# Performance work log

Measured on AMD Instinct MI355X. Metric: run time of the kernel, lower is better.

Reference implementation:

```python
import jax, jax.numpy as jnp
import numpy as np

N_NODES = 50000
N_EDGES = 800000
IN_FEAT = 128
OUT_FEAT = 128


def _glorot(key, shape):
    fan_in, fan_out = shape[1], shape[0]
    lim = jnp.sqrt(6.0 / (fan_in + fan_out))
    return jax.random.uniform(key, shape, jnp.float32, -lim, lim)


def setup_inputs() -> dict:
    key = jax.random.key(0)
    ks = jax.random.split(key, 9)
    x = jax.random.normal(ks[0], (N_NODES, IN_FEAT), jnp.float32)
    edge_index = jax.random.randint(ks[1], (2, N_EDGES), 0, N_NODES, jnp.int64)
    # SAGEConv params: lin_l applied to aggregated neighbors (with bias),
    # lin_r applied to root features (no bias) -- PyG default mean aggregation.
    W1l = _glorot(ks[2], (OUT_FEAT, IN_FEAT)); b1l = jnp.zeros((OUT_FEAT,), jnp.float32)
    W1r = _glorot(ks[3], (OUT_FEAT, IN_FEAT))
    W2l = _glorot(ks[4], (OUT_FEAT, OUT_FEAT)); b2l = jnp.zeros((OUT_FEAT,), jnp.float32)
    W2r = _glorot(ks[5], (OUT_FEAT, OUT_FEAT))
    Wlin = _glorot(ks[6], (2, OUT_FEAT)); blin = jnp.zeros((2,), jnp.float32)
    return {"x": x, "edge_index": edge_index,
            "W1l": W1l, "b1l": b1l, "W1r": W1r,
            "W2l": W2l, "b2l": b2l, "W2r": W2r,
            "Wlin": Wlin, "blin": blin}


def _sage_conv(x, src, dst, Wl, bl, Wr, n_nodes):
    # mean-aggregate neighbor features at destination nodes
    agg_sum = jax.ops.segment_sum(x[src], dst, num_segments=n_nodes)  # [N, F]
    deg = jax.ops.segment_sum(jnp.ones((src.shape[0],), x.dtype), dst, num_segments=n_nodes)
    agg = agg_sum / jnp.maximum(deg, 1.0)[:, None]
    return agg @ Wl.T + bl + x @ Wr.T


def reference(x, edge_index, W1l, b1l, W1r, W2l, b2l, W2r, Wlin, blin):
    src, dst = edge_index[0], edge_index[1]
    n = x.shape[0]
    h = _sage_conv(x, src, dst, W1l, b1l, W1r, n)
    h = jax.nn.relu(h)  # dropout is identity in eval mode
    h = _sage_conv(h, src, dst, W2l, b2l, W2r, n)
    h = jax.nn.relu(h)
    logits = h @ Wlin.T + blin  # [N, 2]
    return jax.nn.log_softmax(logits, axis=1)
```

## Files before the change

### kernel.cpp

```cpp
#include <hip/hip_runtime.h>
#include <math.h>

#define N_NODES 50000
#define N_EDGES 800000
#define F 128
#define ELL_CAP 64
#define NSHARD 8
#define RANKS 128
#define EPR (N_EDGES / RANKS)
#define NPS (N_NODES / NSHARD)
#define NBPS 25
#define NBUCK (NSHARD * NBPS)
#define BIN_CAP 80
#define BUCK_CAP 4608
#define EDGE_BLKS (NSHARD * RANKS)
#define CVT_BLKS 6250

typedef __attribute__((ext_vector_type(8))) short short8;
typedef __attribute__((ext_vector_type(4))) float float4v;

__device__ inline unsigned short f2bf(float f) {
    unsigned int u = __builtin_bit_cast(unsigned int, f);
    u += 0x7FFF + ((u >> 16) & 1);
    return (unsigned short)(u >> 16);
}
__device__ inline float bf2f_lo(unsigned int u) {
    return __builtin_bit_cast(float, u << 16);
}
__device__ inline float bf2f_hi(unsigned int u) {
    return __builtin_bit_cast(float, u & 0xFFFF0000u);
}
__device__ inline float i8f(unsigned int u, int k) {
    return (float)((signed char)(u >> (k * 8)));
}

__global__ __launch_bounds__(256) void prep1(const float* __restrict__ x,
                                             const int* __restrict__ src,
                                             const int* __restrict__ dst,
                                             const float* __restrict__ W1l,
                                             const float* __restrict__ W1r,
                                             const float* __restrict__ W2l,
                                             const float* __restrict__ W2r,
                                             unsigned short* __restrict__ xb,
                                             unsigned char* __restrict__ xq,
                                             float* __restrict__ xscale,
                                             int* __restrict__ tails,
                                             unsigned int* __restrict__ bucketEdges,
                                             unsigned short* __restrict__ P1,
                                             unsigned short* __restrict__ P2) {
    int blk = blockIdx.x;
    int tid = threadIdx.x;
    if (blk < EDGE_BLKS) {
        __shared__ int bin_cnt[NBPS];
        __shared__ int bin_base[NBPS];
        __shared__ unsigned int bins[NBPS * BIN_CAP];
        int shard = blk & 7;
        int rank = blk >> 3;
        int lo = shard * NPS;
        if (tid < NBPS) bin_cnt[tid] = 0;
        __syncthreads();
        int base = rank * EPR;
        for (int i = tid; i < EPR; i += 256) {
            int d = dst[base + i];
            unsigned int du = (unsigned int)(d - lo);
            if (du < (unsigned int)NPS) {
                int s = src[base + i];
                int lb = du >> 8;
                int pos = atomicAdd(&bin_cnt[lb], 1);
                if (pos < BIN_CAP)
                    bins[lb * BIN_CAP + pos] = ((du & 255u) << 16) | (unsigned int)s;
            }
        }
        __syncthreads();
        if (tid < NBPS) {
            int c = bin_cnt[tid]; if (c > BIN_CAP) c = BIN_CAP;
            bin_cnt[tid] = c;
            bin_base[tid] = atomicAdd(&tails[shard * NBPS + tid], c);
        }
        __syncthreads();
        for (int b2 = 0; b2 < NBPS; ++b2) {
            int c = bin_cnt[b2];
            int rb = bin_base[b2];
            unsigned int* dp = bucketEdges + (size_t)(shard * NBPS + b2) * BUCK_CAP;
            for (int i = tid; i < c; i += 256)
                if (rb + i < BUCK_CAP) dp[rb + i] = bins[b2 * BIN_CAP + i];
        }
    } else if (blk < EDGE_BLKS + CVT_BLKS) {
        int row = (blk - EDGE_BLKS) * 8 + (tid >> 5);
        int hl = tid & 31;
        float4 v = ((const float4*)x)[row * 32 + hl];
        float m = fmaxf(fmaxf(fabsf(v.x), fabsf(v.y)), fmaxf(fabsf(v.z), fabsf(v.w)));
        #pragma unroll
        for (int off = 1; off < 32; off <<= 1) m = fmaxf(m, __shfl_xor(m, off));
        float inv = m > 0.f ? 127.f / m : 0.f;
        int q0 = (int)rintf(v.x * inv), q1 = (int)rintf(v.y * inv);
        int q2 = (int)rintf(v.z * inv), q3 = (int)rintf(v.w * inv);
        unsigned int qp = (q0 & 255) | ((q1 & 255) << 8) | ((q2 & 255) << 16) | ((q3 & 255) << 24);
        ((unsigned int*)xq)[row * 32 + hl] = qp;
        unsigned int p0 = (unsigned int)f2bf(v.x) | ((unsigned int)f2bf(v.y) << 16);
        unsigned int p1 = (unsigned int)f2bf(v.z) | ((unsigned int)f2bf(v.w) << 16);
        ((uint2*)xb)[row * 32 + hl] = make_uint2(p0, p1);
        if (hl == 0) xscale[row] = m * (1.f / 127.f);
    } else {
        int pblk = blk - (EDGE_BLKS + CVT_BLKS);
        int t = (pblk & 15) * 256 + tid;
        int lane = t & 63;
        int ct = (t >> 6) & 7;
        int ks = t >> 9;
        const float* Wl = (pblk < 16) ? W1l : W2l;
        const float* Wr = (pblk < 16) ? W1r : W2r;
        unsigned short* P = (pblk < 16) ? P1 : P2;
        int col = ct * 16 + (lane & 15);
        int kbase = (ks & 3) * 32 + (lane >> 4) * 8;
        const float* W = (ks < 4) ? Wl : Wr;
        unsigned short* dp = P + (size_t)t * 8;
        #pragma unroll
        for (int j = 0; j < 8; ++j) dp[j] = f2bf(W[col * F + kbase + j]);
    }
}

__global__ __launch_bounds__(256) void ell_build(const int* __restrict__ tails,
                                                 const unsigned int* __restrict__ bucketEdges,
                                                 int* __restrict__ cnt,
                                                 unsigned short* __restrict__ nbr) {
    __shared__ int cl[256];
    __shared__ unsigned short ell[256 * ELL_CAP];
    int b = blockIdx.x;
    int tid = threadIdx.x;
    cl[tid] = 0;
    __syncthreads();
    int T = tails[b]; if (T > BUCK_CAP) T = BUCK_CAP;
    const unsigned int* eb = bucketEdges + (size_t)b * BUCK_CAP;
    for (int i = tid; i < T; i += 256) {
        unsigned int rec = eb[i];
        int nib = rec >> 16;
        int pos = atomicAdd(&cl[nib], 1);
        if (pos < ELL_CAP) ell[nib * ELL_CAP + pos] = (unsigned short)(rec & 0xFFFFu);
    }
    __syncthreads();
    int shard = b / NBPS, lb = b % NBPS;
    int nb0 = shard * NPS + lb * 256;
    int nn = NPS - lb * 256; if (nn > 256) nn = 256;
    if (tid < nn) cnt[nb0 + tid] = cl[tid];
    const uint4* s4 = (const uint4*)ell;
    uint4* d4 = (uint4*)(nbr + (size_t)nb0 * ELL_CAP);
    int n4 = nn * (ELL_CAP * 2 / 16);
    for (int i = tid; i < n4; i += 256) d4[i] = s4[i];
}

__global__ __launch_bounds__(256) void aggregate_q(const unsigned char* __restrict__ Xq,
                                                   const float* __restrict__ xs,
                                                   const int* __restrict__ cnt,
                                                   const unsigned short* __restrict__ nbr,
                                                   unsigned short* __restrict__ agg) {
    int tid = threadIdx.x;
    int wave = tid >> 6;
    int lane = tid & 63;
    int half = lane >> 5;
    int hl = lane & 31;
    int node = blockIdx.x * 8 + wave * 2 + half;

    int degt = cnt[node];
    int deg = degt < ELL_CAP ? degt : ELL_CAP;
    const unsigned short* nb = nbr + node * ELL_CAP;
    const unsigned int* Xu = (const unsigned int*)Xq;

    float a0 = 0.f, a1 = 0.f, a2 = 0.f, a3 = 0.f;
    int s = 0;
    for (; s + 4 <= deg; s += 4) {
        ushort4 nv = *(const ushort4*)(nb + s);
        unsigned int g0 = Xu[nv.x * 32 + hl]; float s0 = xs[nv.x];
        unsigned int g1 = Xu[nv.y * 32 + hl]; float s1 = xs[nv.y];
        unsigned int g2 = Xu[nv.z * 32 + hl]; float s2 = xs[nv.z];
        unsigned int g3 = Xu[nv.w * 32 + hl]; float s3 = xs[nv.w];
        a0 += i8f(g0, 0) * s0 + i8f(g1, 0) * s1 + i8f(g2, 0) * s2 + i8f(g3, 0) * s3;
        a1 += i8f(g0, 1) * s0 + i8f(g1, 1) * s1 + i8f(g2, 1) * s2 + i8f(g3, 1) * s3;
        a2 += i8f(g0, 2) * s0 + i8f(g1, 2) * s1 + i8f(g2, 2) * s2 + i8f(g3, 2) * s3;
        a3 += i8f(g0, 3) * s0 + i8f(g1, 3) * s1 + i8f(g2, 3) * s2 + i8f(g3, 3) * s3;
    }
    for (; s < deg; ++s) {
        int v = nb[s];
        unsigned int g = Xu[v * 32 + hl]; float sc = xs[v];
        a0 += i8f(g, 0) * sc; a1 += i8f(g, 1) * sc;
        a2 += i8f(g, 2) * sc; a3 += i8f(g, 3) * sc;
    }
    float inv = 1.0f / (float)(degt > 0 ? degt : 1);
    unsigned int p0 = (unsigned int)f2bf(a0 * inv) | ((unsigned int)f2bf(a1 * inv) << 16);
    unsigned int p1 = (unsigned int)f2bf(a2 * inv) | ((unsigned int)f2bf(a3 * inv) << 16);
    *(uint2*)(agg + (size_t)node * F + hl * 4) = make_uint2(p0, p1);
}

__global__ __launch_bounds__(256) void sage_gemm(const unsigned short* __restrict__ Abf,
                                                 const unsigned short* __restrict__ Bbf,
                                                 const unsigned short* __restrict__ Pw,
                                                 const float* __restrict__ bias,
                                                 unsigned short* __restrict__ Hout,
                                                 unsigned char* __restrict__ Hq,
                                                 float* __restrict__ Hscale,
                                                 const float* __restrict__ Wlin,
                                                 const float* __restrict__ blin,
                                                 float* __restrict__ out, int mode) {
    int lane = threadIdx.x & 63;
    int wave = threadIdx.x >> 6;
    int r0 = blockIdx.x * 64 + wave * 16;
    int rowA = r0 + (lane & 15);
    if (rowA >= N_NODES) rowA = N_NODES - 1;
    int kg = lane >> 4;

    short8 af[4], bfr[4];
    const short8* Ap = (const short8*)(Abf + (size_t)rowA * F);
    const short8* Bp = (const short8*)(Bbf + (size_t)rowA * F);
    #pragma unroll
    for (int ks = 0; ks < 4; ++ks) {
        af[ks]  = Ap[ks * 4 + kg];
        bfr[ks] = Bp[ks * 4 + kg];
    }

    const short8* Wp = (const short8*)Pw;
    float4v acc[8];
    #pragma unroll
    for (int ct = 0; ct < 8; ++ct) {
        float4v c = {0.f, 0.f, 0.f, 0.f};
        #pragma unroll
        for (int ks = 0; ks < 4; ++ks)
            c = __builtin_amdgcn_mfma_f32_16x16x32_bf16(af[ks], Wp[(ks * 8 + ct) * 64 + lane], c, 0, 0, 0);
        #pragma unroll
        for (int ks = 0; ks < 4; ++ks)
            c = __builtin_amdgcn_mfma_f32_16x16x32_bf16(bfr[ks], Wp[((ks + 4) * 8 + ct) * 64 + lane], c, 0, 0, 0);
        acc[ct] = c;
    }

    int colb = lane & 15;
    int rq = lane >> 4;
    #pragma unroll
    for (int ct = 0; ct < 8; ++ct) {
        float bv = bias[ct * 16 + colb];
        #pragma unroll
        for (int i = 0; i < 4; ++i)
            acc[ct][i] = fmaxf(acc[ct][i] + bv, 0.f);
    }

    if (mode == 0) {
        #pragma unroll
        for (int ct = 0; ct < 8; ++ct) {
            #pragma unroll
            for (int i = 0; i < 4; ++i) {
                int row = r0 + rq * 4 + i;
                if (row < N_NODES)
                    Hout[(size_t)row * F + ct * 16 + colb] = f2bf(acc[ct][i]);
            }
        }
        #pragma unroll
        for (int i = 0; i < 4; ++i) {
            float m = 0.f;
            #pragma unroll
            for (int ct = 0; ct < 8; ++ct) m = fmaxf(m, acc[ct][i]);
            #pragma unroll
            for (int off = 1; off < 16; off <<= 1) m = fmaxf(m, __shfl_xor(m, off));
            float inv = m > 0.f ? 127.f / m : 0.f;
            int row = r0 + rq * 4 + i;
            if (row < N_NODES) {
                if (colb == 0) Hscale[row] = m * (1.f / 127.f);
                #pragma unroll
                for (int ct = 0; ct < 8; ++ct) {
                    int q = (int)rintf(acc[ct][i] * inv);
                    Hq[(size_t)row * F + ct * 16 + colb] = (unsigned char)q;
                }
            }
        }
    } else {
        float w0[8], w1[8];
        #pragma unroll
        for (int ct = 0; ct < 8; ++ct) {
            w0[ct] = Wlin[ct * 16 + colb];
            w1[ct] = Wlin[F + ct * 16 + colb];
        }
        #pragma unroll
        for (int i = 0; i < 4; ++i) {
            float p0 = 0.f, p1 = 0.f;
            #pragma unroll
            for (int ct = 0; ct < 8; ++ct) {
                p0 += acc[ct][i] * w0[ct];
                p1 += acc[ct][i] * w1[ct];
            }
            #pragma unroll
            for (int off = 1; off < 16; off <<= 1) {
                p0 += __shfl_xor(p0, off);
                p1 += __shfl_xor(p1, off);
            }
            int row = r0 + rq * 4 + i;
            if (colb == 0 && row < N_NODES) {
                float a = p0 + blin[0];
                float b = p1 + blin[1];
                float m = fmaxf(a, b);
                float lse = m + logf(expf(a - m) + expf(b - m));
                out[(size_t)row * 2 + 0] = a - lse;
                out[(size_t)row * 2 + 1] = b - lse;
            }
        }
    }
}

extern "C" void kernel_launch(void* const* d_in, const int* in_sizes, int n_in,
                              void* d_out, int out_size, void* d_ws, size_t ws_size,
                              hipStream_t stream) {
    const float* x    = (const float*)d_in[0];
    const int*   ei   = (const int*)d_in[1];
    const float* W1l  = (const float*)d_in[2];
    const float* b1l  = (const float*)d_in[3];
    const float* W1r  = (const float*)d_in[4];
    const float* W2l  = (const float*)d_in[5];
    const float* b2l  = (const float*)d_in[6];
    const float* W2r  = (const float*)d_in[7];
    const float* Wlin = (const float*)d_in[8];
    const float* blin = (const float*)d_in[9];
    float* out = (float*)d_out;

    const int* src = ei;
    const int* dst = ei + N_EDGES;

    char* ws = (char*)d_ws;
    int*            tails  = (int*)ws;
    unsigned int*   bEdge  = (unsigned int*)(ws + 4096);
    int*            cnt    = (int*)(ws + 3694592);
    unsigned short* nbr    = (unsigned short*)(ws + 3895296);
    unsigned short* xb     = (unsigned short*)(ws + 10296320);
    unsigned short* h1b    = (unsigned short*)(ws + 23097344);
    unsigned short* aggb   = (unsigned short*)(ws + 35898368);
    unsigned short* P1     = (unsigned short*)(ws + 48699392);
    unsigned short* P2     = (unsigned short*)(ws + 48764928);
    unsigned char*  xq     = (unsigned char*)(ws + 48830464);
    unsigned char*  h1q    = (unsigned char*)(ws + 55230464);
    float*          xscale = (float*)(ws + 61630464);
    float*          h1scale= (float*)(ws + 61830464);

    hipMemsetAsync(tails, 0, NBUCK * sizeof(int), stream);

    prep1<<<EDGE_BLKS + CVT_BLKS + 32, 256, 0, stream>>>(x, src, dst, W1l, W1r, W2l, W2r,
                                                         xb, xq, xscale, tails, bEdge, P1, P2);
    ell_build<<<NBUCK, 256, 0, stream>>>(tails, bEdge, cnt, nbr);

    aggregate_q<<<6250, 256, 0, stream>>>(xq, xscale, cnt, nbr, aggb);
    sage_gemm<<<782, 256, 0, stream>>>(aggb, xb, P1, b1l, h1b, h1q, h1scale,
                                       nullptr, nullptr, nullptr, 0);

    aggregate_q<<<6250, 256, 0, stream>>>(h1q, h1scale, cnt, nbr, aggb);
    sage_gemm<<<782, 256, 0, stream>>>(aggb, h1b, P2, b2l, nullptr, nullptr, nullptr,
                                       Wlin, blin, out, 1);
}
```

Measured before the change: 127.6 us.

## Replace sharded edge bucketing with single-pass global binning over all buckets

Edge bucketing used to run as 8 shards × 128 ranks, so every block re-read its slice of the edge list and kept only the edges whose destinations fell in its shard. Each edge was therefore read eight times. Now 125 blocks each read a contiguous edge chunk once and bin every edge into one of 196 global 256-node buckets, held in a larger shared-memory staging area. Each bucket's bins are then flushed by a single thread with a serial loop, which removes the redundant global reads. In exchange there are far fewer edge blocks, more LDS per block, and uncoalesced serial flush stores that may lengthen the critical path of the prep kernel.

```diff
diff --git a/kernel.cpp b/kernel.cpp
--- a/kernel.cpp
+++ b/kernel.cpp
@@ -5,15 +5,11 @@
 #define N_EDGES 800000
 #define F 128
 #define ELL_CAP 64
-#define NSHARD 8
-#define RANKS 128
-#define EPR (N_EDGES / RANKS)
-#define NPS (N_NODES / NSHARD)
-#define NBPS 25
-#define NBUCK (NSHARD * NBPS)
-#define BIN_CAP 80
+#define NBUCK 196
+#define BIN_CAP 97
 #define BUCK_CAP 4608
-#define EDGE_BLKS (NSHARD * RANKS)
+#define EDGE_BLKS 125
+#define EPR (N_EDGES / EDGE_BLKS)
 #define CVT_BLKS 6250
 
 typedef __attribute__((ext_vector_type(8))) short short8;
@@ -51,39 +47,28 @@
     int blk = blockIdx.x;
     int tid = threadIdx.x;
     if (blk < EDGE_BLKS) {
-        __shared__ int bin_cnt[NBPS];
-        __shared__ int bin_base[NBPS];
-        __shared__ unsigned int bins[NBPS * BIN_CAP];
-        int shard = blk & 7;
-        int rank = blk >> 3;
-        int lo = shard * NPS;
-        if (tid < NBPS) bin_cnt[tid] = 0;
+        __shared__ int bin_cnt[NBUCK];
+        __shared__ unsigned int bins[NBUCK * BIN_CAP];
+        for (int i = tid; i < NBUCK; i += 256) bin_cnt[i] = 0;
         __syncthreads();
-        int base = rank * EPR;
+        int base = blk * EPR;
         for (int i = tid; i < EPR; i += 256) {
             int d = dst[base + i];
-            unsigned int du = (unsigned int)(d - lo);
-            if (du < (unsigned int)NPS) {
-                int s = src[base + i];
-                int lb = du >> 8;
-                int pos = atomicAdd(&bin_cnt[lb], 1);
-                if (pos < BIN_CAP)
-                    bins[lb * BIN_CAP + pos] = ((du & 255u) << 16) | (unsigned int)s;
-            }
+            int s = src[base + i];
+            int lb = d >> 8;
+            int pos = atomicAdd(&bin_cnt[lb], 1);
+            if (pos < BIN_CAP)
+                bins[lb * BIN_CAP + pos] = ((unsigned int)(d & 255) << 16) | (unsigned int)s;
         }
         __syncthreads();
-        if (tid < NBPS) {
+        if (tid < NBUCK) {
             int c = bin_cnt[tid]; if (c > BIN_CAP) c = BIN_CAP;
-            bin_cnt[tid] = c;
-            bin_base[tid] = atomicAdd(&tails[shard * NBPS + tid], c);
-        }
-        __syncthreads();
-        for (int b2 = 0; b2 < NBPS; ++b2) {
-            int c = bin_cnt[b2];
-            int rb = bin_base[b2];
-            unsigned int* dp = bucketEdges + (size_t)(shard * NBPS + b2) * BUCK_CAP;
-            for (int i = tid; i < c; i += 256)
-                if (rb + i < BUCK_CAP) dp[rb + i] = bins[b2 * BIN_CAP + i];
+            int rb = atomicAdd(&tails[tid], c);
+            unsigned int* dp = bucketEdges + (size_t)tid * BUCK_CAP;
+            for (int i = 0; i < c; ++i) {
+                int p = rb + i;
+                if (p < BUCK_CAP) dp[p] = bins[tid * BIN_CAP + i];
+            }
         }
     } else if (blk < EDGE_BLKS + CVT_BLKS) {
         int row = (blk - EDGE_BLKS) * 8 + (tid >> 5);
@@ -138,9 +123,8 @@
         if (pos < ELL_CAP) ell[nib * ELL_CAP + pos] = (unsigned short)(rec & 0xFFFFu);
     }
     __syncthreads();
-    int shard = b / NBPS, lb = b % NBPS;
-    int nb0 = shard * NPS + lb * 256;
-    int nn = NPS - lb * 256; if (nn > 256) nn = 256;
+    int nb0 = b * 256;
+    int nn = N_NODES - nb0; if (nn > 256) nn = 256;
     if (tid < nn) cnt[nb0 + tid] = cl[tid];
     const uint4* s4 = (const uint4*)ell;
     uint4* d4 = (uint4*)(nbr + (size_t)nb0 * ELL_CAP);
@@ -322,17 +306,17 @@
     char* ws = (char*)d_ws;
     int*            tails  = (int*)ws;
     unsigned int*   bEdge  = (unsigned int*)(ws + 4096);
-    int*            cnt    = (int*)(ws + 3694592);
-    unsigned short* nbr    = (unsigned short*)(ws + 3895296);
-    unsigned short* xb     = (unsigned short*)(ws + 10296320);
-    unsigned short* h1b    = (unsigned short*)(ws + 23097344);
-    unsigned short* aggb   = (unsigned short*)(ws + 35898368);
-    unsigned short* P1     = (unsigned short*)(ws + 48699392);
-    unsigned short* P2     = (unsigned short*)(ws + 48764928);
-    unsigned char*  xq     = (unsigned char*)(ws + 48830464);
-    unsigned char*  h1q    = (unsigned char*)(ws + 55230464);
-    float*          xscale = (float*)(ws + 61630464);
-    float*          h1scale= (float*)(ws + 61830464);
+    int*            cnt    = (int*)(ws + 3620864);
+    unsigned short* nbr    = (unsigned short*)(ws + 3821568);
+    unsigned short* xb     = (unsigned short*)(ws + 10221568);
+    unsigned short* h1b    = (unsigned short*)(ws + 23021568);
+    unsigned short* aggb   = (unsigned short*)(ws + 35821568);
+    unsigned short* P1     = (unsigned short*)(ws + 48621568);
+    unsigned short* P2     = (unsigned short*)(ws + 48687104);
+    unsigned char*  xq     = (unsigned char*)(ws + 48752640);
+    unsigned char*  h1q    = (unsigned char*)(ws + 55152640);
+    float*          xscale = (float*)(ws + 61552640);
+    float*          h1scale= (float*)(ws + 61752640);
 
     hipMemsetAsync(tails, 0, NBUCK * sizeof(int), stream);
 
```

Result: faster. 122.1 us (-4.3%).
